# Optimization experiments

Measured on AMD Instinct MI355X. Metric: run time of the kernel, lower is better.

## Reference

```python
import jax, jax.numpy as jnp
import numpy as np

N_NODES = 100000
N_EDGES = 1200000
D_FEAT = 64


def setup_inputs() -> dict:
    key = jax.random.key(0)
    k1, k2, k3 = jax.random.split(key, 3)
    x = jax.random.normal(k1, (N_NODES, D_FEAT), dtype=jnp.float32)
    edge_index = jax.random.randint(k2, (2, N_EDGES), 0, N_NODES, dtype=jnp.int64)
    edge_weight = jax.random.uniform(k3, (N_EDGES, 1), dtype=jnp.float32)
    return {"x": x, "edge_index": edge_index, "edge_weight": edge_weight}


def reference(x, edge_index, edge_weight):
    # flow = source_to_target: j = edge_index[0] (source), i = edge_index[1] (target)
    src, dst = edge_index[0], edge_index[1]
    # message: x_j  (gather along node_dim=-2)
    msg = x[src]                       # [E, D]
    # aggregate: scatter-'sum' with edge_weight scaling
    msg = msg * edge_weight            # [E, D]
    out = jax.ops.segment_sum(msg, dst, num_segments=N_NODES)  # [N, D]
    # update: identity
    return out
```

## Files before the change

### kernel.cpp

```cpp
#include <hip/hip_runtime.h>
#include <hip/hip_bf16.h>


constexpr int D_FEAT        = 64;
constexpr int BIN_SHIFT     = 6;
constexpr int NODES_PER_BIN = 1 << BIN_SHIFT;
constexpr int NBINS_MAX     = 2048;
constexpr int BIN_CAP       = 1024;
constexpr int EPB           = 4096;
constexpr int OVF_CAP       = 32768;

__device__ __forceinline__ int wave_incl_scan(int v, int lane) {
    #pragma unroll
    for (int d = 1; d < 64; d <<= 1) {
        int t = __shfl_up(v, d);
        if (lane >= d) v += t;
    }
    return v;
}

__device__ __forceinline__ unsigned short f32_to_bf16_rn(float f) {
    unsigned int u = __float_as_uint(f);
    u += 0x7FFFu + ((u >> 16) & 1u);
    return (unsigned short)(u >> 16);
}

__global__ __launch_bounds__(1024) void mp_partition(
    const int* __restrict__ src, const int* __restrict__ dst,
    const float* __restrict__ w, const float* __restrict__ x,
    ushort* __restrict__ xb, int n4,
    int*  __restrict__ gcnt,
    int2* __restrict__ payload,
    int*  __restrict__ ovf_cnt, int4* __restrict__ ovf,
    int n_edges, int nbins)
{
    __shared__ int cnt[NBINS_MAX];
    __shared__ int start[NBINS_MAX];
    __shared__ int cur[NBINS_MAX];
    __shared__ int gbase[NBINS_MAX];
    __shared__ unsigned short binof[EPB];
    __shared__ int2 sorted[EPB];
    __shared__ int wsum[16];

    const int t    = threadIdx.x;
    const int lane = t & 63;
    const int wid  = t >> 6;
    const int base = blockIdx.x * EPB;
    const int nblk = min(EPB, n_edges - base);

    cnt[t] = 0;
    cnt[t + 1024] = 0;

    const int i4 = (base >> 2) + t;
    const bool have = (i4 * 4 < n_edges);
    int4 d4 = make_int4(0, 0, 0, 0);
    if (have) d4 = reinterpret_cast<const int4*>(dst)[i4];

    for (int i = blockIdx.x * 1024 + t; i < n4; i += gridDim.x * 1024) {
        const float4 v = reinterpret_cast<const float4*>(x)[i];
        ushort4 o;
        o.x = f32_to_bf16_rn(v.x);
        o.y = f32_to_bf16_rn(v.y);
        o.z = f32_to_bf16_rn(v.z);
        o.w = f32_to_bf16_rn(v.w);
        reinterpret_cast<ushort4*>(xb)[i] = o;
    }
    __syncthreads();

    if (have) {
        atomicAdd(&cnt[d4.x >> BIN_SHIFT], 1);
        atomicAdd(&cnt[d4.y >> BIN_SHIFT], 1);
        atomicAdd(&cnt[d4.z >> BIN_SHIFT], 1);
        atomicAdd(&cnt[d4.w >> BIN_SHIFT], 1);
    }
    __syncthreads();

    {
        const int base0 = wid * 128;
        const int c0 = cnt[base0 + lane];
        const int c1 = cnt[base0 + 64 + lane];
        const int s0_ = wave_incl_scan(c0, lane);
        const int t0  = __shfl(s0_, 63);
        const int s1_ = wave_incl_scan(c1, lane) + t0;
        if (lane == 63) wsum[wid] = s1_;

        for (int k = t; k < nbins; k += 1024) {
            const int c = cnt[k];
            if (c > 0) gbase[k] = atomicAdd(&gcnt[k], c);
        }
        __syncthreads();

        int cpre = 0;
        #pragma unroll
        for (int k = 0; k < 16; ++k) cpre += (k < wid) ? wsum[k] : 0;
        const int e0 = cpre + s0_ - c0;
        const int e1 = cpre + s1_ - c1;
        start[base0 + lane]      = e0;  cur[base0 + lane]      = e0;
        start[base0 + 64 + lane] = e1;  cur[base0 + 64 + lane] = e1;
    }
    __syncthreads();

    if (have) {
        const int4   s4 = reinterpret_cast<const int4*>(src)[i4];
        const float4 w4 = reinterpret_cast<const float4*>(w)[i4];
        const int   dd[4] = {d4.x, d4.y, d4.z, d4.w};
        const int   ss[4] = {s4.x, s4.y, s4.z, s4.w};
        const float ww[4] = {w4.x, w4.y, w4.z, w4.w};
        #pragma unroll
        for (int j = 0; j < 4; ++j) {
            const int b   = dd[j] >> BIN_SHIFT;
            const int low = dd[j] & (NODES_PER_BIN - 1);
            const int p   = atomicAdd(&cur[b], 1);
            sorted[p] = make_int2((low << 20) | ss[j], __float_as_int(ww[j]));
            binof[p]  = (unsigned short)b;
        }
    }
    __syncthreads();

    #pragma unroll
    for (int k = 0; k < EPB / 1024; ++k) {
        const int i = k * 1024 + t;
        if (i >= nblk) break;
        const int b    = binof[i];
        const int idx  = i - start[b];
        const int gpos = gbase[b] + idx;
        const int2 e   = sorted[i];
        if (gpos < BIN_CAP) {
            payload[(size_t)b * BIN_CAP + gpos] = e;
        } else {
            const int op = atomicAdd(ovf_cnt, 1);
            if (op < OVF_CAP)
                ovf[op] = make_int4((b << BIN_SHIFT) + (e.x >> 20),
                                    e.x & 0xFFFFF, e.y, 0);
        }
    }
}


#define ACC8(XV, WW) do {                                          \
    a0 = fmaf(__uint_as_float((XV).x << 16),         (WW), a0);    \
    a1 = fmaf(__uint_as_float((XV).x & 0xFFFF0000u), (WW), a1);    \
    a2 = fmaf(__uint_as_float((XV).y << 16),         (WW), a2);    \
    a3 = fmaf(__uint_as_float((XV).y & 0xFFFF0000u), (WW), a3);    \
    a4 = fmaf(__uint_as_float((XV).z << 16),         (WW), a4);    \
    a5 = fmaf(__uint_as_float((XV).z & 0xFFFF0000u), (WW), a5);    \
    a6 = fmaf(__uint_as_float((XV).w << 16),         (WW), a6);    \
    a7 = fmaf(__uint_as_float((XV).w & 0xFFFF0000u), (WW), a7);    \
} while (0)

__global__ __launch_bounds__(256) void mp_bin_gather(
    const ushort* __restrict__ xb,
    const float*  __restrict__ x,
    const int*  __restrict__ gcnt,
    const int2* __restrict__ payload,
    const int*  __restrict__ ovf_cnt, const int4* __restrict__ ovf,
    float* __restrict__ out, int n_nodes)
{
    __shared__ int2 sraw[BIN_CAP];
    __shared__ int2 sedge[BIN_CAP];
    __shared__ int ncnt[NODES_PER_BIN];
    __shared__ int nstart[NODES_PER_BIN + 1];
    __shared__ int ncur[NODES_PER_BIN];

    const int b    = blockIdx.x;
    const int t    = threadIdx.x;
    const int wid  = t >> 6;
    const int lane = t & 63;
    const int sub  = lane >> 3;
    const int fq   = lane & 7;
    const int fg   = fq * 8;

    const int m = min(gcnt[b], BIN_CAP);
    const int2* pl = payload + (size_t)b * BIN_CAP;

    if (t < NODES_PER_BIN) ncnt[t] = 0;
    __syncthreads();

    for (int i = t; i < m; i += 256) {
        const int2 e = pl[i];
        sraw[i] = e;
        atomicAdd(&ncnt[e.x >> 20], 1);
    }
    __syncthreads();

    if (t < 64) {
        const int c0 = ncnt[t];
        const int s0_ = wave_incl_scan(c0, t);
        nstart[t] = s0_ - c0;
        ncur[t]   = s0_ - c0;
        if (t == 63) nstart[64] = s0_;
    }
    __syncthreads();

    for (int i = t; i < m; i += 256) {
        const int2 e = sraw[i];
        const int p  = atomicAdd(&ncur[e.x >> 20], 1);
        sedge[p] = e;
    }
    __syncthreads();

    const int novf = *ovf_cnt;

    #define XROW(SRC) (*reinterpret_cast<const uint4*>(xb + (size_t)(SRC) * D_FEAT + fg))

    #pragma unroll
    for (int nb = 0; nb < 16; nb += 8) {
        const int n    = wid * 16 + nb + sub;
        const int node = (b << BIN_SHIFT) + n;
        const int s0 = nstart[n];
        const int s1 = nstart[n + 1];

        float a0 = 0.f, a1 = 0.f, a2 = 0.f, a3 = 0.f;
        float a4 = 0.f, a5 = 0.f, a6 = 0.f, a7 = 0.f;

        int e = s0;
        for (; e + 4 <= s1; e += 4) {
            const int2 pA = sedge[e];
            const int2 pB = sedge[e + 1];
            const int2 pC = sedge[e + 2];
            const int2 pD = sedge[e + 3];
            const uint4 xA = XROW(pA.x & 0xFFFFF);
            const uint4 xB = XROW(pB.x & 0xFFFFF);
            const uint4 xC = XROW(pC.x & 0xFFFFF);
            const uint4 xD = XROW(pD.x & 0xFFFFF);
            const float wA = __int_as_float(pA.y);
            const float wB = __int_as_float(pB.y);
            const float wC = __int_as_float(pC.y);
            const float wD = __int_as_float(pD.y);
            ACC8(xA, wA);
            ACC8(xB, wB);
            ACC8(xC, wC);
            ACC8(xD, wD);
        }
        if (e + 2 <= s1) {
            const int2 pA = sedge[e];
            const int2 pB = sedge[e + 1];
            const uint4 xA = XROW(pA.x & 0xFFFFF);
            const uint4 xB = XROW(pB.x & 0xFFFFF);
            const float wA = __int_as_float(pA.y);
            const float wB = __int_as_float(pB.y);
            ACC8(xA, wA);
            ACC8(xB, wB);
            e += 2;
        }
        if (e < s1) {
            const int2 p = sedge[e];
            const uint4 xv = XROW(p.x & 0xFFFFF);
            const float ww = __int_as_float(p.y);
            ACC8(xv, ww);
        }

        if (node < n_nodes) {
            if (novf > 0) {
                const int lim = min(novf, OVF_CAP);
                for (int j = 0; j < lim; ++j) {
                    const int4 o = ovf[j];
                    if (o.x == node) {
                        const float* xr = x + (size_t)o.y * D_FEAT + fg;
                        const float ww = __int_as_float(o.z);
                        a0 = fmaf(xr[0], ww, a0); a1 = fmaf(xr[1], ww, a1);
                        a2 = fmaf(xr[2], ww, a2); a3 = fmaf(xr[3], ww, a3);
                        a4 = fmaf(xr[4], ww, a4); a5 = fmaf(xr[5], ww, a5);
                        a6 = fmaf(xr[6], ww, a6); a7 = fmaf(xr[7], ww, a7);
                    }
                }
            }
            float* orow = out + (size_t)node * D_FEAT + fg;
            *reinterpret_cast<float4*>(orow)     = make_float4(a0, a1, a2, a3);
            *reinterpret_cast<float4*>(orow + 4) = make_float4(a4, a5, a6, a7);
        }
    }
    #undef XROW
}

__global__ __launch_bounds__(256) void mp_scatter_atomic(
    const float* __restrict__ x, const int* __restrict__ src,
    const int* __restrict__ dst, const float* __restrict__ w,
    float* __restrict__ out, int n_edges)
{
    const int gtid = blockIdx.x * blockDim.x + threadIdx.x;
    const int edge = gtid >> 6;
    const int lane = threadIdx.x & 63;
    if (edge >= n_edges) return;
    const int s = src[edge];
    const int d = dst[edge];
    const float ww = w[edge];
    atomicAdd(&out[(size_t)d * D_FEAT + lane], x[(size_t)s * D_FEAT + lane] * ww);
}

extern "C" void kernel_launch(void* const* d_in, const int* in_sizes, int n_in,
                              void* d_out, int out_size, void* d_ws, size_t ws_size,
                              hipStream_t stream)
{
    const float* x          = (const float*)d_in[0];
    const int*   edge_index = (const int*)d_in[1];
    const float* w          = (const float*)d_in[2];
    float*       out        = (float*)d_out;

    const int n_edges = in_sizes[1] / 2;
    const int n_nodes = in_sizes[0] / D_FEAT;
    const int* src = edge_index;
    const int* dst = edge_index + n_edges;

    const int nbins = (n_nodes + NODES_PER_BIN - 1) >> BIN_SHIFT;

    int*    gcnt    = (int*)d_ws;
    int*    ovf_cnt = gcnt + NBINS_MAX;
    int4*   ovf     = (int4*)(gcnt + NBINS_MAX + 64);
    int2*   payload = (int2*)(ovf + OVF_CAP);
    ushort* xb      = (ushort*)(payload + (size_t)nbins * BIN_CAP);
    const size_t need = (size_t)(NBINS_MAX + 64) * 4 + (size_t)OVF_CAP * 16
                      + (size_t)nbins * BIN_CAP * 8
                      + (size_t)n_nodes * D_FEAT * 2;

    const bool ok = (ws_size >= need) && (nbins <= NBINS_MAX) && ((n_edges & 3) == 0)
                 && ((n_nodes * D_FEAT) % 4 == 0) && (n_nodes <= 131072);

    if (ok) {
        hipMemsetAsync(gcnt, 0, (size_t)(NBINS_MAX + 64) * 4, stream);
        const int n4 = n_nodes * D_FEAT / 4;
        const int g1 = (n_edges + EPB - 1) / EPB;
        mp_partition<<<g1, 1024, 0, stream>>>(src, dst, w, x, xb, n4,
                                              gcnt, payload, ovf_cnt, ovf,
                                              n_edges, nbins);
        mp_bin_gather<<<nbins, 256, 0, stream>>>(xb, x, gcnt, payload,
                                                 ovf_cnt, ovf, out, n_nodes);
        return;
    }

    hipMemsetAsync(d_out, 0, (size_t)out_size * sizeof(float), stream);
    const int grid = (int)(((size_t)n_edges * 64 + 255) / 256);
    mp_scatter_atomic<<<grid, 256, 0, stream>>>(x, src, dst, w, out, n_edges);
}
```

Baseline: 125.8 us.

## Widen destination bins to 512 nodes and split each bin across two gather blocks

Destination bins grow from 64 to 512 nodes (196 bins instead of 1563), which shrinks per-block bin bookkeeping and scan work in the partition kernel and makes payload writes per bin larger and more contiguous. The gather kernel now launches two 512-thread blocks per bin. Each block filters the bin's payload by a node-half bit and handles 256 nodes, and the raw staging buffer is dropped. Each gather block reads the whole bin payload twice, and an edge that does not fit the 4096-entry sedge buffer is silently dropped, which is a correctness risk for skewed inputs.

Result: no change. 126.6 us (+0.6%).

```diff
diff --git a/kernel.cpp b/kernel.cpp
--- a/kernel.cpp
+++ b/kernel.cpp
@@ -3,11 +3,12 @@
 
 
 constexpr int D_FEAT        = 64;
-constexpr int BIN_SHIFT     = 6;
+constexpr int BIN_SHIFT     = 9;
 constexpr int NODES_PER_BIN = 1 << BIN_SHIFT;
-constexpr int NBINS_MAX     = 2048;
-constexpr int BIN_CAP       = 1024;
+constexpr int NBINS_MAX     = 256;
+constexpr int BIN_CAP       = 8192;
 constexpr int EPB           = 4096;
+constexpr int SED_CAP       = 4096;
 constexpr int OVF_CAP       = 32768;
 
 __device__ __forceinline__ int wave_incl_scan(int v, int lane) {
@@ -38,18 +39,14 @@
     __shared__ int start[NBINS_MAX];
     __shared__ int cur[NBINS_MAX];
     __shared__ int gbase[NBINS_MAX];
-    __shared__ unsigned short binof[EPB];
+    __shared__ unsigned char binof[EPB];
     __shared__ int2 sorted[EPB];
-    __shared__ int wsum[16];
 
     const int t    = threadIdx.x;
-    const int lane = t & 63;
-    const int wid  = t >> 6;
     const int base = blockIdx.x * EPB;
     const int nblk = min(EPB, n_edges - base);
 
-    cnt[t] = 0;
-    cnt[t + 1024] = 0;
+    if (t < NBINS_MAX) cnt[t] = 0;
 
     const int i4 = (base >> 2) + t;
     const bool have = (i4 * 4 < n_edges);
@@ -75,28 +72,21 @@
     }
     __syncthreads();
 
-    {
-        const int base0 = wid * 128;
-        const int c0 = cnt[base0 + lane];
-        const int c1 = cnt[base0 + 64 + lane];
-        const int s0_ = wave_incl_scan(c0, lane);
-        const int t0  = __shfl(s0_, 63);
-        const int s1_ = wave_incl_scan(c1, lane) + t0;
-        if (lane == 63) wsum[wid] = s1_;
-
-        for (int k = t; k < nbins; k += 1024) {
-            const int c = cnt[k];
-            if (c > 0) gbase[k] = atomicAdd(&gcnt[k], c);
-        }
-        __syncthreads();
-
-        int cpre = 0;
+    if (t < 64) {
+        int carry = 0;
         #pragma unroll
-        for (int k = 0; k < 16; ++k) cpre += (k < wid) ? wsum[k] : 0;
-        const int e0 = cpre + s0_ - c0;
-        const int e1 = cpre + s1_ - c1;
-        start[base0 + lane]      = e0;  cur[base0 + lane]      = e0;
-        start[base0 + 64 + lane] = e1;  cur[base0 + 64 + lane] = e1;
+        for (int k = 0; k < 4; ++k) {
+            const int idx = k * 64 + t;
+            const int c = cnt[idx];
+            const int s = wave_incl_scan(c, t) + carry;
+            start[idx] = s - c;
+            cur[idx]   = s - c;
+            carry = __shfl(s, 63);
+        }
+    }
+    for (int k = t; k < nbins; k += 1024) {
+        const int c = cnt[k];
+        if (c > 0) gbase[k] = atomicAdd(&gcnt[k], c);
     }
     __syncthreads();
 
@@ -112,7 +102,7 @@
             const int low = dd[j] & (NODES_PER_BIN - 1);
             const int p   = atomicAdd(&cur[b], 1);
             sorted[p] = make_int2((low << 20) | ss[j], __float_as_int(ww[j]));
-            binof[p]  = (unsigned short)b;
+            binof[p]  = (unsigned char)b;
         }
     }
     __syncthreads();
@@ -148,7 +138,7 @@
     a7 = fmaf(__uint_as_float((XV).w & 0xFFFF0000u), (WW), a7);    \
 } while (0)
 
-__global__ __launch_bounds__(256) void mp_bin_gather(
+__global__ __launch_bounds__(512) void mp_bin_gather(
     const ushort* __restrict__ xb,
     const float*  __restrict__ x,
     const int*  __restrict__ gcnt,
@@ -156,13 +146,14 @@
     const int*  __restrict__ ovf_cnt, const int4* __restrict__ ovf,
     float* __restrict__ out, int n_nodes)
 {
-    __shared__ int2 sraw[BIN_CAP];
-    __shared__ int2 sedge[BIN_CAP];
-    __shared__ int ncnt[NODES_PER_BIN];
-    __shared__ int nstart[NODES_PER_BIN + 1];
-    __shared__ int ncur[NODES_PER_BIN];
-
-    const int b    = blockIdx.x;
+    __shared__ int2 sedge[SED_CAP];
+    __shared__ int ncnt[256];
+    __shared__ int nstart[257];
+    __shared__ int ncur[256];
+
+    const int bs   = blockIdx.x;
+    const int b    = bs >> 1;
+    const int half = bs & 1;
     const int t    = threadIdx.x;
     const int wid  = t >> 6;
     const int lane = t & 63;
@@ -173,29 +164,37 @@
     const int m = min(gcnt[b], BIN_CAP);
     const int2* pl = payload + (size_t)b * BIN_CAP;
 
-    if (t < NODES_PER_BIN) ncnt[t] = 0;
-    __syncthreads();
-
-    for (int i = t; i < m; i += 256) {
+    if (t < 256) ncnt[t] = 0;
+    __syncthreads();
+
+    for (int i = t; i < m; i += 512) {
+        const int e = pl[i].x;
+        if (((e >> 28) & 1) == half)
+            atomicAdd(&ncnt[(e >> 20) & 255], 1);
+    }
+    __syncthreads();
+
+    if (t < 64) {
+        int carry = 0;
+        #pragma unroll
+        for (int k = 0; k < 4; ++k) {
+            const int idx = k * 64 + t;
+            const int c = ncnt[idx];
+            const int s = wave_incl_scan(c, t) + carry;
+            nstart[idx] = s - c;
+            ncur[idx]   = s - c;
+            carry = __shfl(s, 63);
+        }
+        if (t == 63) nstart[256] = carry;
+    }
+    __syncthreads();
+
+    for (int i = t; i < m; i += 512) {
         const int2 e = pl[i];
-        sraw[i] = e;
-        atomicAdd(&ncnt[e.x >> 20], 1);
-    }
-    __syncthreads();
-
-    if (t < 64) {
-        const int c0 = ncnt[t];
-        const int s0_ = wave_incl_scan(c0, t);
-        nstart[t] = s0_ - c0;
-        ncur[t]   = s0_ - c0;
-        if (t == 63) nstart[64] = s0_;
-    }
-    __syncthreads();
-
-    for (int i = t; i < m; i += 256) {
-        const int2 e = sraw[i];
-        const int p  = atomicAdd(&ncur[e.x >> 20], 1);
-        sedge[p] = e;
+        if (((e.x >> 28) & 1) == half) {
+            const int p = atomicAdd(&ncur[(e.x >> 20) & 255], 1);
+            if (p < SED_CAP) sedge[p] = e;
+        }
     }
     __syncthreads();
 
@@ -204,9 +203,9 @@
     #define XROW(SRC) (*reinterpret_cast<const uint4*>(xb + (size_t)(SRC) * D_FEAT + fg))
 
     #pragma unroll
-    for (int nb = 0; nb < 16; nb += 8) {
-        const int n    = wid * 16 + nb + sub;
-        const int node = (b << BIN_SHIFT) + n;
+    for (int nb = 0; nb < 32; nb += 8) {
+        const int n    = wid * 32 + nb + sub;
+        const int node = (b << BIN_SHIFT) + (half << 8) + n;
         const int s0 = nstart[n];
         const int s1 = nstart[n + 1];
 
@@ -323,8 +322,8 @@
         mp_partition<<<g1, 1024, 0, stream>>>(src, dst, w, x, xb, n4,
                                               gcnt, payload, ovf_cnt, ovf,
                                               n_edges, nbins);
-        mp_bin_gather<<<nbins, 256, 0, stream>>>(xb, x, gcnt, payload,
-                                                 ovf_cnt, ovf, out, n_nodes);
+        mp_bin_gather<<<nbins * 2, 512, 0, stream>>>(xb, x, gcnt, payload,
+                                                     ovf_cnt, ovf, out, n_nodes);
         return;
     }
 
```
